# Kernel optimization log

Measured on AMD Instinct MI355X. Metric: run time of the kernel, lower is better.

## Reference

```python
import jax, jax.numpy as jnp
import numpy as np
from jax import lax

NUM_CLASSES = 19
IGNORE_INDEX = 255
THRESH = 0.7
MIN_KEPT = 100000

N, C, H, W = 8, 19, 512, 1024


def setup_inputs() -> dict:
    key = jax.random.key(0)
    k1, k2 = jax.random.split(key)
    predict = jax.random.normal(k1, (N, C, H, W), dtype=jnp.float32)
    target = jax.random.randint(k2, (N, H, W), 0, NUM_CLASSES, dtype=jnp.int32)
    return {"predict": predict, "target": target}


def _class_weights(flat_lab):
    # get_weights: median(counts)/counts for present classes, 1.0 otherwise.
    ones = jnp.ones(flat_lab.shape, dtype=jnp.float32)
    counts = jnp.zeros((NUM_CLASSES,), jnp.float32).at[flat_lab].add(ones, mode='drop')
    present = counts > 0
    med = jnp.nanmedian(jnp.where(present, counts, jnp.nan))
    return jnp.where(present, med / jnp.maximum(counts, 1.0), 1.0)


def reference(predict, target):
    n, c, h, w = predict.shape
    flat_lab = target.reshape(-1)                       # (P,)
    valid = flat_lab != IGNORE_INDEX                    # (P,)
    num_valid = valid.sum()

    weight = _class_weights(flat_lab)                   # (C,) from ORIGINAL target

    # per-pixel log-softmax over classes
    logits = jnp.transpose(predict, (0, 2, 3, 1)).reshape(-1, c)  # (P, C)
    logp = jax.nn.log_softmax(logits, axis=-1)
    safe_lab = jnp.where(valid, flat_lab, 0)
    logp_true = jnp.take_along_axis(logp, safe_lab[:, None], axis=1)[:, 0]  # (P,)
    pred_prob = jnp.exp(lax.stop_gradient(logp_true))   # prob of true class, detached

    # order-statistic threshold over valid pixels (invalid -> +inf, sorts last)
    pred_sortable = jnp.where(valid, pred_prob, jnp.inf)
    sorted_pred = jnp.sort(pred_sortable)
    k = jnp.minimum(MIN_KEPT, num_valid) - 1
    kth = sorted_pred[jnp.maximum(k, 0)]
    threshold = jnp.where(kth > THRESH, kth, THRESH)

    kept_ohem = valid & (pred_sortable <= threshold)
    do_ohem = num_valid > MIN_KEPT                      # else keep all valid pixels
    kept = jnp.where(do_ohem, kept_ohem, valid)

    # weighted cross entropy over kept pixels (torch 'mean' with class weights)
    wpix = weight[safe_lab] * kept.astype(jnp.float32)
    loss = jnp.sum(wpix * (-logp_true)) / jnp.maximum(jnp.sum(wpix), 1e-12)
    return loss
```

## Files before the change

kernel.cpp:

```cpp
#include <hip/hip_runtime.h>

#define NCLS 19
#define HW_ (512 * 1024)
#define MIN_KEPT_ 100000LL
#define NSLOT 32
#define COARSE_BINS 1280
#define COARSE_BASE 0x3F333u

struct Accums {
    unsigned int coarse[COARSE_BINS];
    unsigned int fine12[4096];
    unsigned int slotCnt[NSLOT][NCLS];
    float        slotSumA[NSLOT][NCLS];
    unsigned int slotCntG[NSLOT][NCLS];
    float        slotSumG[NSLOT][NCLS];
    unsigned int cntR[NCLS];
    float        sumR[NCLS];
    float        weights[NCLS];
    unsigned int flag;
    unsigned int sel_prefix;
    unsigned int rank_rem;
    float        threshold;
    unsigned int done1, done2;
};

__device__ __forceinline__ unsigned int aloadu(const unsigned int* p) {
    return __hip_atomic_load(p, __ATOMIC_RELAXED, __HIP_MEMORY_SCOPE_AGENT);
}
__device__ __forceinline__ float aloadf(const float* p) {
    return __hip_atomic_load(p, __ATOMIC_RELAXED, __HIP_MEMORY_SCOPE_AGENT);
}

__device__ __forceinline__ void accum_pixel(unsigned int* sCnt, float* sSumA,
                                            unsigned int* sCntG, float* sSumG,
                                            Accums* ws, int lab, float logp, float prob) {
    if (lab < 0 || lab >= NCLS) return;
    float nlp = -logp;
    atomicAdd(&sCnt[lab], 1u);
    atomicAdd(&sSumA[lab], nlp);
    if (prob > 0.7f) {
        atomicAdd(&sCntG[lab], 1u);
        atomicAdd(&sSumG[lab], nlp);
        unsigned int bits = __float_as_uint(prob);
        int bin = (int)(bits >> 12) - (int)COARSE_BASE;
        bin = bin < 0 ? 0 : (bin >= COARSE_BINS ? COARSE_BINS - 1 : bin);
        atomicAdd(&ws->coarse[bin], 1u);
    }
}

__device__ __forceinline__ bool pix_logp(const float* __restrict__ pred,
                                         const int* __restrict__ targ,
                                         int p, float& logp, float& prob, int& lab) {
    lab = targ[p];
    if (lab < 0 || lab >= NCLS) return false;
    int n = p / HW_;
    int hw = p - n * HW_;
    const float* pb = pred + (size_t)n * NCLS * HW_ + hw;
    float v[NCLS];
    float mx = -3.4e38f, vt = 0.f;
#pragma unroll
    for (int c = 0; c < NCLS; ++c) {
        float x = pb[(size_t)c * HW_];
        v[c] = x;
        mx = fmaxf(mx, x);
        vt = (lab == c) ? x : vt;
    }
    float s = 0.f;
#pragma unroll
    for (int c = 0; c < NCLS; ++c) s += __expf(v[c] - mx);
    logp = vt - (mx + __logf(s));
    prob = __expf(logp);
    return true;
}

__global__ __launch_bounds__(256) void k_main(const float* __restrict__ pred,
                                              const int* __restrict__ targ,
                                              Accums* __restrict__ ws, int P) {
    __shared__ unsigned int sCnt[NCLS], sCntG[NCLS];
    __shared__ float sSumA[NCLS], sSumG[NCLS];
    if (threadIdx.x < NCLS) {
        sCnt[threadIdx.x] = 0u; sCntG[threadIdx.x] = 0u;
        sSumA[threadIdx.x] = 0.f; sSumG[threadIdx.x] = 0.f;
    }
    __syncthreads();

    int gid = blockIdx.x * blockDim.x + threadIdx.x;
    int p4 = gid * 4;
    if (p4 < P) {
        if (p4 + 3 < P) {
            int n = p4 / HW_;
            int hw = p4 - n * HW_;
            const float* pb = pred + (size_t)n * NCLS * HW_ + hw;
            int4 lab = *reinterpret_cast<const int4*>(targ + p4);
            float4 vv[NCLS];
            float4 mx = make_float4(-3.4e38f, -3.4e38f, -3.4e38f, -3.4e38f);
            float4 vt = make_float4(0.f, 0.f, 0.f, 0.f);
#pragma unroll
            for (int c = 0; c < NCLS; ++c) {
                float4 v = *reinterpret_cast<const float4*>(pb + (size_t)c * HW_);
                vv[c] = v;
                mx.x = fmaxf(mx.x, v.x); mx.y = fmaxf(mx.y, v.y);
                mx.z = fmaxf(mx.z, v.z); mx.w = fmaxf(mx.w, v.w);
                vt.x = (lab.x == c) ? v.x : vt.x;
                vt.y = (lab.y == c) ? v.y : vt.y;
                vt.z = (lab.z == c) ? v.z : vt.z;
                vt.w = (lab.w == c) ? v.w : vt.w;
            }
            float4 s = make_float4(0.f, 0.f, 0.f, 0.f);
#pragma unroll
            for (int c = 0; c < NCLS; ++c) {
                s.x += __expf(vv[c].x - mx.x);
                s.y += __expf(vv[c].y - mx.y);
                s.z += __expf(vv[c].z - mx.z);
                s.w += __expf(vv[c].w - mx.w);
            }
            {
                float lp = vt.x - (mx.x + __logf(s.x));
                accum_pixel(sCnt, sSumA, sCntG, sSumG, ws, lab.x, lp, __expf(lp));
                lp = vt.y - (mx.y + __logf(s.y));
                accum_pixel(sCnt, sSumA, sCntG, sSumG, ws, lab.y, lp, __expf(lp));
                lp = vt.z - (mx.z + __logf(s.z));
                accum_pixel(sCnt, sSumA, sCntG, sSumG, ws, lab.z, lp, __expf(lp));
                lp = vt.w - (mx.w + __logf(s.w));
                accum_pixel(sCnt, sSumA, sCntG, sSumG, ws, lab.w, lp, __expf(lp));
            }
        } else {
            for (int j = 0; j < 4; ++j) {
                int p = p4 + j;
                if (p >= P) break;
                float lp, pr; int lb;
                if (pix_logp(pred, targ, p, lp, pr, lb))
                    accum_pixel(sCnt, sSumA, sCntG, sSumG, ws, lb, lp, pr);
            }
        }
    }
    __syncthreads();
    int slot = blockIdx.x & (NSLOT - 1);
    if (threadIdx.x < NCLS) {
        int i = threadIdx.x;
        if (sCnt[i])          atomicAdd(&ws->slotCnt[slot][i], sCnt[i]);
        if (sSumA[i] != 0.f)  atomicAdd(&ws->slotSumA[slot][i], sSumA[i]);
        if (sCntG[i])         atomicAdd(&ws->slotCntG[slot][i], sCntG[i]);
        if (sSumG[i] != 0.f)  atomicAdd(&ws->slotSumG[slot][i], sSumG[i]);
    }
}

__global__ void k_finalize(Accums* __restrict__ ws, float* __restrict__ out) {
    __shared__ unsigned int cnt[NCLS], cG[NCLS];
    __shared__ float sA[NCLS], sG[NCLS];
    int t = threadIdx.x;
    if (t < NCLS) {
        unsigned int c = 0, cg = 0; float a = 0.f, b = 0.f;
        for (int s = 0; s < NSLOT; ++s) {
            c  += ws->slotCnt[s][t];  a += ws->slotSumA[s][t];
            cg += ws->slotCntG[s][t]; b += ws->slotSumG[s][t];
        }
        cnt[t] = c; cG[t] = cg; sA[t] = a; sG[t] = b;
    }
    __syncthreads();
    if (t != 0) return;

    long long nv = 0, c7tot = 0;
    for (int c = 0; c < NCLS; ++c) { nv += cnt[c]; c7tot += (long long)(cnt[c] - cG[c]); }

    float w[NCLS];
    {
        float vals[NCLS]; int m = 0;
        for (int c = 0; c < NCLS; ++c)
            if (cnt[c] > 0) vals[m++] = (float)cnt[c];
        for (int i = 1; i < m; ++i) {
            float x = vals[i]; int j = i - 1;
            while (j >= 0 && vals[j] > x) { vals[j + 1] = vals[j]; --j; }
            vals[j + 1] = x;
        }
        float med = 1.f;
        if (m > 0) med = (m & 1) ? vals[m / 2] : 0.5f * (vals[m / 2 - 1] + vals[m / 2]);
        for (int c = 0; c < NCLS; ++c) {
            w[c] = (cnt[c] > 0) ? med / fmaxf((float)cnt[c], 1.f) : 1.f;
            ws->weights[c] = w[c];
        }
    }

    if (nv == 0) { out[0] = 0.f; return; }

    bool do_ohem = nv > MIN_KEPT_;
    long long kkeep = nv < MIN_KEPT_ ? nv : MIN_KEPT_;

    float S = 0.f, W = 0.f;
    if (!do_ohem) {
        for (int c = 0; c < NCLS; ++c) { S += w[c] * sA[c]; W += w[c] * (float)cnt[c]; }
    } else if (c7tot >= kkeep) {
        for (int c = 0; c < NCLS; ++c) {
            S += w[c] * (sA[c] - sG[c]);
            W += w[c] * (float)(cnt[c] - cG[c]);
        }
    } else {
        unsigned int r = (unsigned int)(kkeep - c7tot);
        unsigned int cum = 0, before = 0; int bsel = COARSE_BINS - 1;
        for (int i = 0; i < COARSE_BINS; ++i) {
            unsigned int nc = cum + ws->coarse[i];
            if (nc >= r) { bsel = i; before = cum; break; }
            cum = nc;
        }
        ws->sel_prefix = COARSE_BASE + (unsigned int)bsel;
        ws->rank_rem = r - before;
        ws->flag = 1u;
        return;
    }
    out[0] = S / fmaxf(W, 1e-12f);
}

__global__ void k_refine(const float* __restrict__ pred, const int* __restrict__ targ,
                         Accums* __restrict__ ws, int P) {
    __shared__ unsigned int flag; __shared__ unsigned int prefix; __shared__ int sIsLast;
    if (threadIdx.x == 0) { flag = ws->flag; prefix = ws->sel_prefix; }
    __syncthreads();
    if (!flag) return;
    int stride = gridDim.x * blockDim.x;
    for (int p = blockIdx.x * blockDim.x + threadIdx.x; p < P; p += stride) {
        float lp, pr; int lb;
        if (!pix_logp(pred, targ, p, lp, pr, lb)) continue;
        if (pr > 0.7f) {
            unsigned int bits = __float_as_uint(pr);
            if ((bits >> 12) == prefix) atomicAdd(&ws->fine12[bits & 0xFFFu], 1u);
        }
    }
    __syncthreads();
    if (threadIdx.x == 0) {
        __threadfence();
        unsigned int old = __hip_atomic_fetch_add(&ws->done1, 1u, __ATOMIC_ACQ_REL,
                                                  __HIP_MEMORY_SCOPE_AGENT);
        sIsLast = (old == gridDim.x - 1);
    }
    __syncthreads();
    if (sIsLast && threadIdx.x == 0) {
        unsigned int r = ws->rank_rem, cum = 0, low = 4095;
        for (unsigned int i = 0; i < 4096; ++i) {
            cum += aloadu(&ws->fine12[i]);
            if (cum >= r) { low = i; break; }
        }
        ws->threshold = __uint_as_float((prefix << 12) | low);
    }
}

__global__ void k_rare(const float* __restrict__ pred, const int* __restrict__ targ,
                       Accums* __restrict__ ws, float* __restrict__ out, int P) {
    __shared__ unsigned int flag; __shared__ float thr; __shared__ int sIsLast;
    if (threadIdx.x == 0) { flag = ws->flag; thr = ws->threshold; }
    __syncthreads();
    if (!flag) return;
    int stride = gridDim.x * blockDim.x;
    for (int p = blockIdx.x * blockDim.x + threadIdx.x; p < P; p += stride) {
        float lp, pr; int lb;
        if (!pix_logp(pred, targ, p, lp, pr, lb)) continue;
        if (pr <= thr) {
            atomicAdd(&ws->cntR[lb], 1u);
            atomicAdd(&ws->sumR[lb], -lp);
        }
    }
    __syncthreads();
    if (threadIdx.x == 0) {
        __threadfence();
        unsigned int old = __hip_atomic_fetch_add(&ws->done2, 1u, __ATOMIC_ACQ_REL,
                                                  __HIP_MEMORY_SCOPE_AGENT);
        sIsLast = (old == gridDim.x - 1);
    }
    __syncthreads();
    if (sIsLast && threadIdx.x == 0) {
        float S = 0.f, W = 0.f;
        for (int c = 0; c < NCLS; ++c) {
            S += ws->weights[c] * aloadf(&ws->sumR[c]);
            W += ws->weights[c] * (float)aloadu(&ws->cntR[c]);
        }
        out[0] = S / fmaxf(W, 1e-12f);
    }
}

extern "C" void kernel_launch(void* const* d_in, const int* in_sizes, int n_in,
                              void* d_out, int out_size, void* d_ws, size_t ws_size,
                              hipStream_t stream) {
    const float* pred = (const float*)d_in[0];
    const int*   targ = (const int*)d_in[1];
    float*       out  = (float*)d_out;
    int P = in_sizes[1];
    Accums* ws = (Accums*)d_ws;

    hipMemsetAsync(d_ws, 0, sizeof(Accums), stream);

    int blocks = (P + 1023) / 1024;
    k_main<<<blocks, 256, 0, stream>>>(pred, targ, ws, P);
    k_finalize<<<1, 64, 0, stream>>>(ws, out);
    k_refine<<<1024, 256, 0, stream>>>(pred, targ, ws, P);
    k_rare<<<1024, 256, 0, stream>>>(pred, targ, ws, out, P);
}
```

Measured before the change: 447.2 us.

## Fuse finalize into main kernel, merge refine and rare passes, drop max-subtraction

The finalize step now runs in the last block of the main kernel via a completion counter, and the separate refine and rare passes are merged into one pass. That pass accumulates weighted sums below the coarse prefix bin and per-fine-bin counts and sums, so the loss is resolved without a third read of the logits. Softmax no longer subtracts the per-pixel max, and each thread handles 8 pixels instead of 4. This saves one full pass over the prediction tensor and a kernel launch. In exchange it risks overflow in exp for large logits and adds heavier global atomics in the rare pass.

After: 635.0 us. +42.0%, slower.

```diff
diff --git a/kernel.cpp b/kernel.cpp
--- a/kernel.cpp
+++ b/kernel.cpp
@@ -9,19 +9,20 @@
 
 struct Accums {
     unsigned int coarse[COARSE_BINS];
-    unsigned int fine12[4096];
+    unsigned int fineCnt[4096];
+    float        fineW[4096];
+    float        fineWnlp[4096];
     unsigned int slotCnt[NSLOT][NCLS];
     float        slotSumA[NSLOT][NCLS];
     unsigned int slotCntG[NSLOT][NCLS];
     float        slotSumG[NSLOT][NCLS];
-    unsigned int cntR[NCLS];
-    float        sumR[NCLS];
     float        weights[NCLS];
+    float        belowS, belowW;
+    float        base_S, base_W;
     unsigned int flag;
     unsigned int sel_prefix;
     unsigned int rank_rem;
-    float        threshold;
-    unsigned int done1, done2;
+    unsigned int done0, done2;
 };
 
 __device__ __forceinline__ unsigned int aloadu(const unsigned int* p) {
@@ -56,28 +57,25 @@
     int n = p / HW_;
     int hw = p - n * HW_;
     const float* pb = pred + (size_t)n * NCLS * HW_ + hw;
-    float v[NCLS];
-    float mx = -3.4e38f, vt = 0.f;
+    float s = 0.f, vt = 0.f;
 #pragma unroll
     for (int c = 0; c < NCLS; ++c) {
         float x = pb[(size_t)c * HW_];
-        v[c] = x;
-        mx = fmaxf(mx, x);
+        s += __expf(x);
         vt = (lab == c) ? x : vt;
     }
-    float s = 0.f;
-#pragma unroll
-    for (int c = 0; c < NCLS; ++c) s += __expf(v[c] - mx);
-    logp = vt - (mx + __logf(s));
+    logp = vt - __logf(s);
     prob = __expf(logp);
     return true;
 }
 
 __global__ __launch_bounds__(256) void k_main(const float* __restrict__ pred,
                                               const int* __restrict__ targ,
-                                              Accums* __restrict__ ws, int P) {
+                                              Accums* __restrict__ ws,
+                                              float* __restrict__ out, int P) {
     __shared__ unsigned int sCnt[NCLS], sCntG[NCLS];
     __shared__ float sSumA[NCLS], sSumG[NCLS];
+    __shared__ int sIsLast;
     if (threadIdx.x < NCLS) {
         sCnt[threadIdx.x] = 0u; sCntG[threadIdx.x] = 0u;
         sSumA[threadIdx.x] = 0.f; sSumG[threadIdx.x] = 0.f;
@@ -85,48 +83,55 @@
     __syncthreads();
 
     int gid = blockIdx.x * blockDim.x + threadIdx.x;
-    int p4 = gid * 4;
-    if (p4 < P) {
-        if (p4 + 3 < P) {
-            int n = p4 / HW_;
-            int hw = p4 - n * HW_;
+    int p8 = gid * 8;
+    if (p8 < P) {
+        if (p8 + 7 < P) {
+            int n = p8 / HW_;
+            int hw = p8 - n * HW_;
             const float* pb = pred + (size_t)n * NCLS * HW_ + hw;
-            int4 lab = *reinterpret_cast<const int4*>(targ + p4);
-            float4 vv[NCLS];
-            float4 mx = make_float4(-3.4e38f, -3.4e38f, -3.4e38f, -3.4e38f);
-            float4 vt = make_float4(0.f, 0.f, 0.f, 0.f);
+            int4 lab0 = *reinterpret_cast<const int4*>(targ + p8);
+            int4 lab1 = *reinterpret_cast<const int4*>(targ + p8 + 4);
+            float4 s0 = make_float4(0.f, 0.f, 0.f, 0.f);
+            float4 s1 = make_float4(0.f, 0.f, 0.f, 0.f);
+            float4 vt0 = make_float4(0.f, 0.f, 0.f, 0.f);
+            float4 vt1 = make_float4(0.f, 0.f, 0.f, 0.f);
 #pragma unroll
             for (int c = 0; c < NCLS; ++c) {
-                float4 v = *reinterpret_cast<const float4*>(pb + (size_t)c * HW_);
-                vv[c] = v;
-                mx.x = fmaxf(mx.x, v.x); mx.y = fmaxf(mx.y, v.y);
-                mx.z = fmaxf(mx.z, v.z); mx.w = fmaxf(mx.w, v.w);
-                vt.x = (lab.x == c) ? v.x : vt.x;
-                vt.y = (lab.y == c) ? v.y : vt.y;
-                vt.z = (lab.z == c) ? v.z : vt.z;
-                vt.w = (lab.w == c) ? v.w : vt.w;
-            }
-            float4 s = make_float4(0.f, 0.f, 0.f, 0.f);
-#pragma unroll
-            for (int c = 0; c < NCLS; ++c) {
-                s.x += __expf(vv[c].x - mx.x);
-                s.y += __expf(vv[c].y - mx.y);
-                s.z += __expf(vv[c].z - mx.z);
-                s.w += __expf(vv[c].w - mx.w);
-            }
-            {
-                float lp = vt.x - (mx.x + __logf(s.x));
-                accum_pixel(sCnt, sSumA, sCntG, sSumG, ws, lab.x, lp, __expf(lp));
-                lp = vt.y - (mx.y + __logf(s.y));
-                accum_pixel(sCnt, sSumA, sCntG, sSumG, ws, lab.y, lp, __expf(lp));
-                lp = vt.z - (mx.z + __logf(s.z));
-                accum_pixel(sCnt, sSumA, sCntG, sSumG, ws, lab.z, lp, __expf(lp));
-                lp = vt.w - (mx.w + __logf(s.w));
-                accum_pixel(sCnt, sSumA, sCntG, sSumG, ws, lab.w, lp, __expf(lp));
-            }
+                float4 va = *reinterpret_cast<const float4*>(pb + (size_t)c * HW_);
+                float4 vb = *reinterpret_cast<const float4*>(pb + (size_t)c * HW_ + 4);
+                s0.x += __expf(va.x); s0.y += __expf(va.y);
+                s0.z += __expf(va.z); s0.w += __expf(va.w);
+                s1.x += __expf(vb.x); s1.y += __expf(vb.y);
+                s1.z += __expf(vb.z); s1.w += __expf(vb.w);
+                vt0.x = (lab0.x == c) ? va.x : vt0.x;
+                vt0.y = (lab0.y == c) ? va.y : vt0.y;
+                vt0.z = (lab0.z == c) ? va.z : vt0.z;
+                vt0.w = (lab0.w == c) ? va.w : vt0.w;
+                vt1.x = (lab1.x == c) ? vb.x : vt1.x;
+                vt1.y = (lab1.y == c) ? vb.y : vt1.y;
+                vt1.z = (lab1.z == c) ? vb.z : vt1.z;
+                vt1.w = (lab1.w == c) ? vb.w : vt1.w;
+            }
+            float lp;
+            lp = vt0.x - __logf(s0.x);
+            accum_pixel(sCnt, sSumA, sCntG, sSumG, ws, lab0.x, lp, __expf(lp));
+            lp = vt0.y - __logf(s0.y);
+            accum_pixel(sCnt, sSumA, sCntG, sSumG, ws, lab0.y, lp, __expf(lp));
+            lp = vt0.z - __logf(s0.z);
+            accum_pixel(sCnt, sSumA, sCntG, sSumG, ws, lab0.z, lp, __expf(lp));
+            lp = vt0.w - __logf(s0.w);
+            accum_pixel(sCnt, sSumA, sCntG, sSumG, ws, lab0.w, lp, __expf(lp));
+            lp = vt1.x - __logf(s1.x);
+            accum_pixel(sCnt, sSumA, sCntG, sSumG, ws, lab1.x, lp, __expf(lp));
+            lp = vt1.y - __logf(s1.y);
+            accum_pixel(sCnt, sSumA, sCntG, sSumG, ws, lab1.y, lp, __expf(lp));
+            lp = vt1.z - __logf(s1.z);
+            accum_pixel(sCnt, sSumA, sCntG, sSumG, ws, lab1.z, lp, __expf(lp));
+            lp = vt1.w - __logf(s1.w);
+            accum_pixel(sCnt, sSumA, sCntG, sSumG, ws, lab1.w, lp, __expf(lp));
         } else {
-            for (int j = 0; j < 4; ++j) {
-                int p = p4 + j;
+            for (int j = 0; j < 8; ++j) {
+                int p = p8 + j;
                 if (p >= P) break;
                 float lp, pr; int lb;
                 if (pix_logp(pred, targ, p, lp, pr, lb))
@@ -143,31 +148,39 @@
         if (sCntG[i])         atomicAdd(&ws->slotCntG[slot][i], sCntG[i]);
         if (sSumG[i] != 0.f)  atomicAdd(&ws->slotSumG[slot][i], sSumG[i]);
     }
-}
-
-__global__ void k_finalize(Accums* __restrict__ ws, float* __restrict__ out) {
-    __shared__ unsigned int cnt[NCLS], cG[NCLS];
-    __shared__ float sA[NCLS], sG[NCLS];
+    __syncthreads();
+    if (threadIdx.x == 0) {
+        __threadfence();
+        unsigned int old = __hip_atomic_fetch_add(&ws->done0, 1u, __ATOMIC_ACQ_REL,
+                                                  __HIP_MEMORY_SCOPE_AGENT);
+        sIsLast = (old == gridDim.x - 1);
+    }
+    __syncthreads();
+    if (!sIsLast) return;
+
     int t = threadIdx.x;
     if (t < NCLS) {
         unsigned int c = 0, cg = 0; float a = 0.f, b = 0.f;
         for (int s = 0; s < NSLOT; ++s) {
-            c  += ws->slotCnt[s][t];  a += ws->slotSumA[s][t];
-            cg += ws->slotCntG[s][t]; b += ws->slotSumG[s][t];
-        }
-        cnt[t] = c; cG[t] = cg; sA[t] = a; sG[t] = b;
+            c  += aloadu(&ws->slotCnt[s][t]);  a += aloadf(&ws->slotSumA[s][t]);
+            cg += aloadu(&ws->slotCntG[s][t]); b += aloadf(&ws->slotSumG[s][t]);
+        }
+        sCnt[t] = c; sCntG[t] = cg; sSumA[t] = a; sSumG[t] = b;
     }
     __syncthreads();
     if (t != 0) return;
 
     long long nv = 0, c7tot = 0;
-    for (int c = 0; c < NCLS; ++c) { nv += cnt[c]; c7tot += (long long)(cnt[c] - cG[c]); }
+    for (int c = 0; c < NCLS; ++c) {
+        nv += sCnt[c];
+        c7tot += (long long)(sCnt[c] - sCntG[c]);
+    }
 
     float w[NCLS];
     {
         float vals[NCLS]; int m = 0;
         for (int c = 0; c < NCLS; ++c)
-            if (cnt[c] > 0) vals[m++] = (float)cnt[c];
+            if (sCnt[c] > 0) vals[m++] = (float)sCnt[c];
         for (int i = 1; i < m; ++i) {
             float x = vals[i]; int j = i - 1;
             while (j >= 0 && vals[j] > x) { vals[j + 1] = vals[j]; --j; }
@@ -176,7 +189,7 @@
         float med = 1.f;
         if (m > 0) med = (m & 1) ? vals[m / 2] : 0.5f * (vals[m / 2 - 1] + vals[m / 2]);
         for (int c = 0; c < NCLS; ++c) {
-            w[c] = (cnt[c] > 0) ? med / fmaxf((float)cnt[c], 1.f) : 1.f;
+            w[c] = (sCnt[c] > 0) ? med / fmaxf((float)sCnt[c], 1.f) : 1.f;
             ws->weights[c] = w[c];
         }
     }
@@ -188,17 +201,23 @@
 
     float S = 0.f, W = 0.f;
     if (!do_ohem) {
-        for (int c = 0; c < NCLS; ++c) { S += w[c] * sA[c]; W += w[c] * (float)cnt[c]; }
+        for (int c = 0; c < NCLS; ++c) { S += w[c] * sSumA[c]; W += w[c] * (float)sCnt[c]; }
     } else if (c7tot >= kkeep) {
         for (int c = 0; c < NCLS; ++c) {
-            S += w[c] * (sA[c] - sG[c]);
-            W += w[c] * (float)(cnt[c] - cG[c]);
+            S += w[c] * (sSumA[c] - sSumG[c]);
+            W += w[c] * (float)(sCnt[c] - sCntG[c]);
         }
     } else {
+        float bS = 0.f, bW = 0.f;
+        for (int c = 0; c < NCLS; ++c) {
+            bS += w[c] * (sSumA[c] - sSumG[c]);
+            bW += w[c] * (float)(sCnt[c] - sCntG[c]);
+        }
+        ws->base_S = bS; ws->base_W = bW;
         unsigned int r = (unsigned int)(kkeep - c7tot);
         unsigned int cum = 0, before = 0; int bsel = COARSE_BINS - 1;
         for (int i = 0; i < COARSE_BINS; ++i) {
-            unsigned int nc = cum + ws->coarse[i];
+            unsigned int nc = cum + aloadu(&ws->coarse[i]);
             if (nc >= r) { bsel = i; before = cum; break; }
             cum = nc;
         }
@@ -210,52 +229,32 @@
     out[0] = S / fmaxf(W, 1e-12f);
 }
 
-__global__ void k_refine(const float* __restrict__ pred, const int* __restrict__ targ,
-                         Accums* __restrict__ ws, int P) {
-    __shared__ unsigned int flag; __shared__ unsigned int prefix; __shared__ int sIsLast;
+__global__ void k_rare(const float* __restrict__ pred, const int* __restrict__ targ,
+                       Accums* __restrict__ ws, float* __restrict__ out, int P) {
+    __shared__ unsigned int flag, prefix; __shared__ int sIsLast;
+    __shared__ float sW[NCLS];
     if (threadIdx.x == 0) { flag = ws->flag; prefix = ws->sel_prefix; }
     __syncthreads();
     if (!flag) return;
+    if (threadIdx.x < NCLS) sW[threadIdx.x] = ws->weights[threadIdx.x];
+    __syncthreads();
     int stride = gridDim.x * blockDim.x;
     for (int p = blockIdx.x * blockDim.x + threadIdx.x; p < P; p += stride) {
         float lp, pr; int lb;
         if (!pix_logp(pred, targ, p, lp, pr, lb)) continue;
         if (pr > 0.7f) {
             unsigned int bits = __float_as_uint(pr);
-            if ((bits >> 12) == prefix) atomicAdd(&ws->fine12[bits & 0xFFFu], 1u);
-        }
-    }
-    __syncthreads();
-    if (threadIdx.x == 0) {
-        __threadfence();
-        unsigned int old = __hip_atomic_fetch_add(&ws->done1, 1u, __ATOMIC_ACQ_REL,
-                                                  __HIP_MEMORY_SCOPE_AGENT);
-        sIsLast = (old == gridDim.x - 1);
-    }
-    __syncthreads();
-    if (sIsLast && threadIdx.x == 0) {
-        unsigned int r = ws->rank_rem, cum = 0, low = 4095;
-        for (unsigned int i = 0; i < 4096; ++i) {
-            cum += aloadu(&ws->fine12[i]);
-            if (cum >= r) { low = i; break; }
-        }
-        ws->threshold = __uint_as_float((prefix << 12) | low);
-    }
-}
-
-__global__ void k_rare(const float* __restrict__ pred, const int* __restrict__ targ,
-                       Accums* __restrict__ ws, float* __restrict__ out, int P) {
-    __shared__ unsigned int flag; __shared__ float thr; __shared__ int sIsLast;
-    if (threadIdx.x == 0) { flag = ws->flag; thr = ws->threshold; }
-    __syncthreads();
-    if (!flag) return;
-    int stride = gridDim.x * blockDim.x;
-    for (int p = blockIdx.x * blockDim.x + threadIdx.x; p < P; p += stride) {
-        float lp, pr; int lb;
-        if (!pix_logp(pred, targ, p, lp, pr, lb)) continue;
-        if (pr <= thr) {
-            atomicAdd(&ws->cntR[lb], 1u);
-            atomicAdd(&ws->sumR[lb], -lp);
+            unsigned int pf = bits >> 12;
+            float w = sW[lb], nlp = -lp;
+            if (pf < prefix) {
+                atomicAdd(&ws->belowS, w * nlp);
+                atomicAdd(&ws->belowW, w);
+            } else if (pf == prefix) {
+                unsigned int low = bits & 0xFFFu;
+                atomicAdd(&ws->fineCnt[low], 1u);
+                atomicAdd(&ws->fineW[low], w);
+                atomicAdd(&ws->fineWnlp[low], w * nlp);
+            }
         }
     }
     __syncthreads();
@@ -267,10 +266,17 @@
     }
     __syncthreads();
     if (sIsLast && threadIdx.x == 0) {
-        float S = 0.f, W = 0.f;
-        for (int c = 0; c < NCLS; ++c) {
-            S += ws->weights[c] * aloadf(&ws->sumR[c]);
-            W += ws->weights[c] * (float)aloadu(&ws->cntR[c]);
+        unsigned int r = ws->rank_rem, cum = 0;
+        float S = ws->base_S + aloadf(&ws->belowS);
+        float W = ws->base_W + aloadf(&ws->belowW);
+        for (unsigned int i = 0; i < 4096; ++i) {
+            unsigned int c = aloadu(&ws->fineCnt[i]);
+            if (c) {
+                S += aloadf(&ws->fineWnlp[i]);
+                W += aloadf(&ws->fineW[i]);
+                cum += c;
+                if (cum >= r) break;
+            }
         }
         out[0] = S / fmaxf(W, 1e-12f);
     }
@@ -287,9 +293,7 @@
 
     hipMemsetAsync(d_ws, 0, sizeof(Accums), stream);
 
-    int blocks = (P + 1023) / 1024;
-    k_main<<<blocks, 256, 0, stream>>>(pred, targ, ws, P);
-    k_finalize<<<1, 64, 0, stream>>>(ws, out);
-    k_refine<<<1024, 256, 0, stream>>>(pred, targ, ws, P);
+    int blocks = (P + 2047) / 2048;
+    k_main<<<blocks, 256, 0, stream>>>(pred, targ, ws, out, P);
     k_rare<<<1024, 256, 0, stream>>>(pred, targ, ws, out, P);
 }
```
